# Optimization experiments

Measured on AMD Instinct MI355X. Metric: run time of the kernel, lower is better.

Reference implementation:

```python
import jax, jax.numpy as jnp
import numpy as np

VOCAB, EMB, HID, LAT = 32000, 512, 1024, 512
B, T = 32, 128


def setup_inputs() -> dict:
    key = jax.random.key(0)
    ks = jax.random.split(key, 10)
    s = 0.02
    return {
        "latent_vector": jax.random.normal(ks[0], (B, LAT), jnp.float32),
        "target_tokens": jax.random.randint(ks[1], (B, T), 0, VOCAB),
        "emb": jax.random.normal(ks[2], (VOCAB, EMB), jnp.float32) * s,
        "W_lh": jax.random.normal(ks[3], (HID, LAT), jnp.float32) * s,
        "b_lh": jnp.zeros((HID,), jnp.float32),
        "W_ih": jax.random.normal(ks[4], (4 * HID, EMB), jnp.float32) * s,
        "b_ih": jnp.zeros((4 * HID,), jnp.float32),
        "W_hh": jax.random.normal(ks[5], (4 * HID, HID), jnp.float32) * s,
        "b_hh": jnp.zeros((4 * HID,), jnp.float32),
        "W_out": jax.random.normal(ks[6], (VOCAB, HID), jnp.float32) * s,
        "b_out": jnp.zeros((VOCAB,), jnp.float32),
    }


def reference(latent_vector, target_tokens, emb, W_lh, b_lh, W_ih, b_ih, W_hh, b_hh, W_out, b_out):
    # teacher_forcing_ratio = 1.0 (deterministic): input at step t is target_tokens[:, t-1]
    h = latent_vector @ W_lh.T + b_lh            # [B, HID]
    c = jnp.zeros_like(h)
    xs = emb[target_tokens[:, :-1]]              # [B, T-1, EMB]
    xs = jnp.swapaxes(xs, 0, 1)                  # [T-1, B, EMB]

    def step(carry, x):
        h, c = carry
        gates = x @ W_ih.T + b_ih + h @ W_hh.T + b_hh   # [B, 4*HID]
        i, f, g, o = jnp.split(gates, 4, axis=-1)       # PyTorch LSTM gate order
        c = jax.nn.sigmoid(f) * c + jax.nn.sigmoid(i) * jnp.tanh(g)
        h = jax.nn.sigmoid(o) * jnp.tanh(c)
        logits = h @ W_out.T + b_out                    # [B, VOCAB]
        return (h, c), logits

    _, logits = jax.lax.scan(step, (h, c), xs)          # [T-1, B, VOCAB]
    return jnp.swapaxes(logits, 0, 1)                   # [B, T-1, VOCAB]
```

## Files before the change

### kernel.cpp

```cpp
#include <hip/hip_runtime.h>
#include <cstdint>

typedef __bf16 bf16x8 __attribute__((ext_vector_type(8)));
typedef __bf16 bf16x4 __attribute__((ext_vector_type(4)));
typedef float  f32x4  __attribute__((ext_vector_type(4)));

#define VOCAB 32000
#define EMB   512
#define HID   1024
#define LAT   512
#define BATCH 32
#define TSTEP 127
#define MROWS 4064
#define MPAD  4096
#define G4    4096
#define NBLK  128
#define NTM   32
#define NTN   250
#define FSTRIDE 64

__device__ __forceinline__ float sigf(float x){ return 1.0f / (1.0f + __expf(-x)); }
__device__ __forceinline__ float tanhfast(float x){
    float ax = fabsf(x);
    float e  = __expf(-2.0f * ax);
    float t  = (1.0f - e) / (1.0f + e);
    return copysignf(t, x);
}

__device__ __forceinline__ void gll16(void* lds, const void* gsrc){
    __builtin_amdgcn_global_load_lds(
        (const __attribute__((address_space(1))) unsigned int*)gsrc,
        (__attribute__((address_space(3))) unsigned int*)lds,
        16, 0, 0);
}

__global__ __launch_bounds__(256) void init_kernel(
    const float* __restrict__ latent,
    const float* __restrict__ Wlh,
    const float* __restrict__ blh,
    __bf16* __restrict__ h0,
    __bf16* __restrict__ Hall,
    unsigned* __restrict__ flags,
    const float* __restrict__ Whh,
    __bf16* __restrict__ Whhb)
{
    if (blockIdx.x >= 128){
        const int n4 = G4 * HID / 4;
        for (int i = (blockIdx.x - 128) * 256 + threadIdx.x; i < n4; i += 64 * 256){
            float4 v = ((const float4*)Whh)[i];
            bf16x4 o = { (__bf16)v.x, (__bf16)v.y, (__bf16)v.z, (__bf16)v.w };
            ((bf16x4*)Whhb)[i] = o;
        }
        return;
    }
    if (blockIdx.x == 0 && threadIdx.x < NBLK)
        flags[threadIdx.x * FSTRIDE] = 0u;

    int id = blockIdx.x * 256 + threadIdx.x;
    int b = id >> 10, j = id & 1023;
    float s = blh[j];
    const float4* lr = (const float4*)(latent + (size_t)b * LAT);
    const float4* wr = (const float4*)(Wlh + (size_t)j * LAT);
    for (int k = 0; k < LAT / 4; ++k){
        float4 a = lr[k], w = wr[k];
        s += a.x * w.x + a.y * w.y + a.z * w.z + a.w * w.w;
    }
    h0[id] = (__bf16)s;
    Hall[(size_t)MROWS * HID + id] = (__bf16)0.0f;
}

__global__ __launch_bounds__(256) void gemm_xg(
    const float* __restrict__ emb,
    const float* __restrict__ Wih,
    const int*   __restrict__ tok,
    float*       __restrict__ xg,
    const float* __restrict__ bih,
    const float* __restrict__ bhh)
{
    __shared__ __bf16 As[2][128 * 32];
    __shared__ __bf16 Bs[2][128 * 32];

    const int tid  = threadIdx.x;
    const int wid  = tid >> 6, lane = tid & 63;
    const int tile_n = blockIdx.x, tile_m = blockIdx.y;
    const int wr = wid >> 1, wc = wid & 1;

    f32x4 acc[4][4] = {};

    auto stage = [&](int kt, int buf){
        #pragma unroll
        for (int j = 0; j < 2; ++j){
            const int slot = tid + j * 256;
            const int row  = slot >> 2;
            const int kb   = kt * 32 + (slot & 3) * 8;
            {
                const int brow = tile_n * 128 + row;
                const float4* p = (const float4*)(Wih + (size_t)brow * EMB + kb);
                float4 u = p[0], v = p[1];
                bf16x8 w = { (__bf16)u.x, (__bf16)u.y, (__bf16)u.z, (__bf16)u.w,
                             (__bf16)v.x, (__bf16)v.y, (__bf16)v.z, (__bf16)v.w };
                *(bf16x8*)&Bs[buf][row * 32 + (slot & 3) * 8] = w;
            }
            {
                int r = tile_m * 128 + row;
                int rc = (r < MROWS) ? r : (MROWS - 1);
                int token = tok[(rc & 31) * 128 + (rc >> 5)];
                const float4* p = (const float4*)(emb + (size_t)token * EMB + kb);
                float4 u = p[0], v = p[1];
                bf16x8 w = { (__bf16)u.x, (__bf16)u.y, (__bf16)u.z, (__bf16)u.w,
                             (__bf16)v.x, (__bf16)v.y, (__bf16)v.z, (__bf16)v.w };
                *(bf16x8*)&As[buf][row * 32 + (slot & 3) * 8] = w;
            }
        }
    };

    const int KT = EMB / 32;
    stage(0, 0);
    for (int kt = 0; kt < KT; ++kt){
        const int buf = kt & 1;
        __syncthreads();
        if (kt + 1 < KT) stage(kt + 1, buf ^ 1);
        const __bf16* Abuf = As[buf];
        const __bf16* Bbuf = Bs[buf];
        const int ar = lane & 15, ko = (lane >> 4) * 8;
        bf16x8 av[4], bv[4];
        #pragma unroll
        for (int m = 0; m < 4; ++m)
            av[m] = *(const bf16x8*)&Abuf[(wr * 64 + m * 16 + ar) * 32 + ko];
        #pragma unroll
        for (int n = 0; n < 4; ++n)
            bv[n] = *(const bf16x8*)&Bbuf[(wc * 64 + n * 16 + ar) * 32 + ko];
        #pragma unroll
        for (int m = 0; m < 4; ++m)
            #pragma unroll
            for (int n = 0; n < 4; ++n)
                acc[m][n] = __builtin_amdgcn_mfma_f32_16x16x32_bf16(av[m], bv[n], acc[m][n], 0, 0, 0);
    }

    const int r0 = tile_m * 128 + wr * 64 + ((lane >> 4) << 2);
    const int c0 = tile_n * 128 + wc * 64 + (lane & 15);
    #pragma unroll
    for (int m = 0; m < 4; ++m){
        #pragma unroll
        for (int n = 0; n < 4; ++n){
            const int col = c0 + n * 16;
            float badd = bih[col] + bhh[col];
            #pragma unroll
            for (int q = 0; q < 4; ++q){
                int row = r0 + m * 16 + q;
                xg[(size_t)row * G4 + col] = acc[m][n][q] + badd;
            }
        }
    }
}

template<int BF16B>
__global__ __launch_bounds__(256) void gemm_logits(
    const __bf16* __restrict__ A,
    const float*  __restrict__ Bf,
    const __bf16* __restrict__ Bb,
    float*        __restrict__ C,
    const float*  __restrict__ bias)
{
    __shared__ __bf16 As[2][128 * 32];
    __shared__ __bf16 Bs[2][128 * 32];

    const int tid  = threadIdx.x;
    const int wid  = tid >> 6, lane = tid & 63;
    const int bid = blockIdx.x;
    const int s   = (bid & 7) * (NTM * NTN / 8) + (bid >> 3);
    const int g   = s / (8 * NTN), rem = s % (8 * NTN);
    const int tile_m = g * 8 + (rem & 7);
    const int tile_n = rem >> 3;
    const int wr = wid >> 1, wc = wid & 1;

    f32x4 acc[4][4] = {};

    auto stage = [&](int kt, int buf){
        const int kb = kt * 32 + (lane & 3) * 8;
        #pragma unroll
        for (int c2 = 0; c2 < 2; ++c2){
            int rA = tile_m * 128 + c2 * 64 + wid * 16 + (lane >> 2);
            gll16(&As[buf][c2 * 2048 + wid * 512], A + (size_t)rA * HID + kb);
            if constexpr (BF16B){
                int rB = tile_n * 128 + c2 * 64 + wid * 16 + (lane >> 2);
                gll16(&Bs[buf][c2 * 2048 + wid * 512], Bb + (size_t)rB * HID + kb);
            }
        }
        if constexpr (!BF16B){
            #pragma unroll
            for (int j = 0; j < 2; ++j){
                const int slot = tid + j * 256;
                const int row  = slot >> 2;
                const int kb2  = kt * 32 + (slot & 3) * 8;
                const int brow = tile_n * 128 + row;
                const float4* p = (const float4*)(Bf + (size_t)brow * HID + kb2);
                float4 u = p[0], v = p[1];
                bf16x8 w = { (__bf16)u.x, (__bf16)u.y, (__bf16)u.z, (__bf16)u.w,
                             (__bf16)v.x, (__bf16)v.y, (__bf16)v.z, (__bf16)v.w };
                *(bf16x8*)&Bs[buf][row * 32 + (slot & 3) * 8] = w;
            }
        }
    };

    const int KT = HID / 32;
    stage(0, 0);
    for (int kt = 0; kt < KT; ++kt){
        const int buf = kt & 1;
        __syncthreads();
        if (kt + 1 < KT) stage(kt + 1, buf ^ 1);
        const __bf16* Abuf = As[buf];
        const __bf16* Bbuf = Bs[buf];
        const int ar = lane & 15, ko = (lane >> 4) * 8;
        bf16x8 av[4], bv[4];
        #pragma unroll
        for (int m = 0; m < 4; ++m)
            av[m] = *(const bf16x8*)&Abuf[(wr * 64 + m * 16 + ar) * 32 + ko];
        #pragma unroll
        for (int n = 0; n < 4; ++n)
            bv[n] = *(const bf16x8*)&Bbuf[(wc * 64 + n * 16 + ar) * 32 + ko];
        #pragma unroll
        for (int m = 0; m < 4; ++m)
            #pragma unroll
            for (int n = 0; n < 4; ++n)
                acc[m][n] = __builtin_amdgcn_mfma_f32_16x16x32_bf16(av[m], bv[n], acc[m][n], 0, 0, 0);
    }

    const int r0 = tile_m * 128 + wr * 64 + ((lane >> 4) << 2);
    const int c0 = tile_n * 128 + wc * 64 + (lane & 15);
    #pragma unroll
    for (int m = 0; m < 4; ++m){
        #pragma unroll
        for (int n = 0; n < 4; ++n){
            const int col = c0 + n * 16;
            float badd = bias[col];
            #pragma unroll
            for (int q = 0; q < 4; ++q){
                int row = r0 + m * 16 + q;
                if (row < MROWS){
                    int t = row >> 5, b = row & 31;
                    __builtin_nontemporal_store(acc[m][n][q] + badd,
                        &C[((size_t)b * TSTEP + t) * VOCAB + col]);
                }
            }
        }
    }
}

__global__ __launch_bounds__(256) void lstm_coop(
    const float*  __restrict__ xg,
    __bf16*       __restrict__ Hall,
    __bf16*       __restrict__ hbuf,
    const __bf16* __restrict__ Whhb,
    unsigned*     __restrict__ flags,
    const float*  __restrict__ Woutf,
    __bf16*       __restrict__ Woutb)
{
    if (blockIdx.x >= NBLK){
        if (Woutb){
            const int n4 = VOCAB * HID / 4;
            for (int i = (blockIdx.x - NBLK) * 256 + threadIdx.x; i < n4; i += NBLK * 256){
                float4 v = ((const float4*)Woutf)[i];
                bf16x4 o = { (__bf16)v.x, (__bf16)v.y, (__bf16)v.z, (__bf16)v.w };
                ((bf16x4*)Woutb)[i] = o;
            }
        }
        return;
    }

    __shared__ float lds_g[4 * 4 * 4 * 64];
    const int tid = threadIdx.x, wid = tid >> 6, lane = tid & 63;
    const int jb = blockIdx.x * 8;

    bf16x8 bfrag[2][8];
    {
        const int gl = lane & 15, ko = (lane >> 4) * 8;
        #pragma unroll
        for (int nt = 0; nt < 2; ++nt){
            int gg = nt * 16 + gl;
            const __bf16* base =
                Whhb + (size_t)((gg >> 3) * HID + jb + (gg & 7)) * HID + wid * 256 + ko;
            #pragma unroll
            for (int ks = 0; ks < 8; ++ks)
                bfrag[nt][ks] = *(const bf16x8*)(base + ks * 32);
        }
    }

    const int b2 = tid >> 2, up0 = (tid & 3) * 2;
    const int mt2 = b2 >> 4, r2 = b2 & 15, reg2 = r2 & 3, lb2 = (r2 >> 2) << 4;
    float cst[2] = {0.0f, 0.0f};

    const float* xq = xg + (size_t)b2 * G4 + jb + up0;
    float2 xv[4];
    if (tid < 128){
        #pragma unroll
        for (int g = 0; g < 4; ++g) xv[g] = *(const float2*)(xq + g * HID);
    }

    const size_t e0 = (size_t)(lane & 15) * HID + wid * 256 + (lane >> 4) * 8;

    for (int t = 0; t < TSTEP; ++t){
        const unsigned long long* hq =
            (const unsigned long long*)(hbuf + (size_t)(t & 1) * (BATCH * HID));
        union { unsigned long long q[2]; bf16x8 v; } xa[16];
        #pragma unroll
        for (int ks = 0; ks < 8; ++ks){
            size_t q0 = (e0 + (size_t)ks * 32) >> 2;
            size_t q1 = q0 + ((size_t)16 * HID >> 2);
            xa[ks].q[0]     = __hip_atomic_load(hq + q0,     __ATOMIC_RELAXED, __HIP_MEMORY_SCOPE_AGENT);
            xa[ks].q[1]     = __hip_atomic_load(hq + q0 + 1, __ATOMIC_RELAXED, __HIP_MEMORY_SCOPE_AGENT);
            xa[8 + ks].q[0] = __hip_atomic_load(hq + q1,     __ATOMIC_RELAXED, __HIP_MEMORY_SCOPE_AGENT);
            xa[8 + ks].q[1] = __hip_atomic_load(hq + q1 + 1, __ATOMIC_RELAXED, __HIP_MEMORY_SCOPE_AGENT);
        }
        f32x4 a00 = {}, a01 = {}, a10 = {}, a11 = {};
        #pragma unroll
        for (int ks = 0; ks < 8; ++ks){
            a00 = __builtin_amdgcn_mfma_f32_16x16x32_bf16(xa[ks].v,     bfrag[0][ks], a00, 0, 0, 0);
            a01 = __builtin_amdgcn_mfma_f32_16x16x32_bf16(xa[ks].v,     bfrag[1][ks], a01, 0, 0, 0);
            a10 = __builtin_amdgcn_mfma_f32_16x16x32_bf16(xa[8 + ks].v, bfrag[0][ks], a10, 0, 0, 0);
            a11 = __builtin_amdgcn_mfma_f32_16x16x32_bf16(xa[8 + ks].v, bfrag[1][ks], a11, 0, 0, 0);
        }
        #pragma unroll
        for (int q = 0; q < 4; ++q){
            lds_g[((0 * 4 + wid) * 4 + q) * 64 + lane] = a00[q];
            lds_g[((1 * 4 + wid) * 4 + q) * 64 + lane] = a01[q];
            lds_g[((2 * 4 + wid) * 4 + q) * 64 + lane] = a10[q];
            lds_g[((3 * 4 + wid) * 4 + q) * 64 + lane] = a11[q];
        }
        __syncthreads();

        unsigned pku = 0;
        if (tid < 128){
            const float* xn = xq + (size_t)(t + 1) * (BATCH * G4);
            float2 xnew[4];
            #pragma unroll
            for (int g = 0; g < 4; ++g) xnew[g] = *(const float2*)(xn + g * HID);

            float h2[2];
            #pragma unroll
            for (int du = 0; du < 2; ++du){
                int u2 = up0 + du;
                float gate[4];
                #pragma unroll
                for (int ty = 0; ty < 4; ++ty){
                    int gg = ty * 8 + u2;
                    int mtnt = mt2 * 2 + (gg >> 4);
                    int li = lb2 | (gg & 15);
                    float s = 0.0f;
                    #pragma unroll
                    for (int w = 0; w < 4; ++w)
                        s += lds_g[((mtnt * 4 + w) * 4 + reg2) * 64 + li];
                    gate[ty] = s;
                }
                float gi = gate[0] + ((du == 0) ? xv[0].x : xv[0].y);
                float gf = gate[1] + ((du == 0) ? xv[1].x : xv[1].y);
                float gc = gate[2] + ((du == 0) ? xv[2].x : xv[2].y);
                float go = gate[3] + ((du == 0) ? xv[3].x : xv[3].y);
                float c = sigf(gf) * cst[du] + sigf(gi) * tanhfast(gc);
                cst[du] = c;
                h2[du] = sigf(go) * tanhfast(c);
            }
            #pragma unroll
            for (int g = 0; g < 4; ++g) xv[g] = xnew[g];

            union { __bf16 h[2]; unsigned u; } pk;
            pk.h[0] = (__bf16)h2[0]; pk.h[1] = (__bf16)h2[1];
            pku = pk.u;
            unsigned* hw = (unsigned*)(hbuf + (size_t)((t + 1) & 1) * (BATCH * HID)
                                       + (size_t)b2 * HID + jb + up0);
            __hip_atomic_store(hw, pku, __ATOMIC_RELAXED, __HIP_MEMORY_SCOPE_AGENT);
        }

        if (t + 1 == TSTEP){
            if (tid < 128)
                *(unsigned*)(Hall + ((size_t)t * BATCH + b2) * HID + jb + up0) = pku;
            break;
        }

        __syncthreads();
        if (tid == 0)
            __hip_atomic_store(&flags[blockIdx.x * FSTRIDE], (unsigned)(t + 1),
                               __ATOMIC_RELAXED, __HIP_MEMORY_SCOPE_AGENT);
        if (tid < 128)
            *(unsigned*)(Hall + ((size_t)t * BATCH + b2) * HID + jb + up0) = pku;
        if (wid == 0){
            const unsigned tgt = (unsigned)(t + 1);
            for (;;){
                unsigned f0 = __hip_atomic_load(&flags[lane * FSTRIDE],
                                  __ATOMIC_RELAXED, __HIP_MEMORY_SCOPE_AGENT);
                unsigned f1 = __hip_atomic_load(&flags[(lane + 64) * FSTRIDE],
                                  __ATOMIC_RELAXED, __HIP_MEMORY_SCOPE_AGENT);
                if (f0 >= tgt && f1 >= tgt) break;
                __builtin_amdgcn_s_sleep(1);
            }
        }
        __syncthreads();
    }
}

extern "C" void kernel_launch(void* const* d_in, const int* in_sizes, int n_in,
                              void* d_out, int out_size, void* d_ws, size_t ws_size,
                              hipStream_t stream)
{
    const float* latent = (const float*)d_in[0];
    const int*   tokens = (const int*)d_in[1];
    const float* emb    = (const float*)d_in[2];
    const float* Wlh    = (const float*)d_in[3];
    const float* blh    = (const float*)d_in[4];
    const float* Wih    = (const float*)d_in[5];
    const float* bih    = (const float*)d_in[6];
    const float* Whh    = (const float*)d_in[7];
    const float* bhh    = (const float*)d_in[8];
    const float* Wout   = (const float*)d_in[9];
    const float* bout   = (const float*)d_in[10];
    float* out = (float*)d_out;

    const size_t xg_b   = (size_t)MPAD * G4 * 4;
    const size_t hall_b = (size_t)MPAD * HID * 2;
    const size_t whh_b  = (size_t)G4 * HID * 2;
    const size_t wout_b = (size_t)VOCAB * HID * 2;
    const size_t hb_b   = (size_t)2 * BATCH * HID * 2;
    const size_t cnt_b  = (size_t)NBLK * FSTRIDE * 4;

    char* p = (char*)d_ws;
    const bool wsA = ws_size >= xg_b + hall_b + whh_b + wout_b + hb_b + cnt_b;
    const bool wsB = ws_size >= hall_b + whh_b + wout_b + hb_b + cnt_b;

    float* xg;
    if (wsA){ xg = (float*)p; p += xg_b; }
    else    { xg = (float*)d_out; }
    __bf16* Hall = (__bf16*)p; p += hall_b;
    __bf16* Whhb = (__bf16*)p; p += whh_b;
    __bf16* Woutb = nullptr;
    if (wsA || wsB){ Woutb = (__bf16*)p; p += wout_b; }
    __bf16* hbuf = (__bf16*)p; p += hb_b;
    unsigned* flags = (unsigned*)p; p += cnt_b;

    init_kernel<<<dim3(192), dim3(256), 0, stream>>>(
        latent, Wlh, blh, hbuf, Hall, flags, Whh, Whhb);

    gemm_xg<<<dim3(G4 / 128, MPAD / 128), dim3(256), 0, stream>>>(
        emb, Wih, tokens, xg, bih, bhh);

    {
        const float*  xgc   = xg;
        __bf16*       hallp = Hall;
        __bf16*       hbp   = hbuf;
        const __bf16* whhp  = Whhb;
        unsigned*     flagp = flags;
        const float*  wof   = Wout;
        __bf16*       wob   = Woutb;
        void* args[] = { (void*)&xgc, (void*)&hallp, (void*)&hbp, (void*)&whhp,
                         (void*)&flagp, (void*)&wof, (void*)&wob };
        hipLaunchCooperativeKernel((void*)lstm_coop, dim3(2 * NBLK), dim3(256),
                                   args, 0, stream);
    }

    if (Woutb)
        gemm_logits<1><<<dim3(NTM * NTN), dim3(256), 0, stream>>>(
            Hall, (const float*)nullptr, Woutb, out, bout);
    else
        gemm_logits<0><<<dim3(NTM * NTN), dim3(256), 0, stream>>>(
            Hall, Wout, (const __bf16*)nullptr, out, bout);
}
```

Before: 1.214 ms.

## Add 256x256-tile 8-wave logits GEMM with 4-stage async LDS pipeline

Replaces the 128x128-tile logits GEMM with a 512-thread kernel computing 256x256 output tiles. It uses a 4-slot global_load_lds ring, split A/B staging interleaved with the MFMA phases, and s_setprio around the MFMA bursts. Blocks are remapped so that blocks sharing A row tiles are grouped, and output is written with nontemporal stores. The larger tiles raise arithmetic intensity and cut L2/HBM re-reads, at the cost of more registers, 64KB of LDS and a tail wave on 2000 blocks. The old kernel stays as a fallback if the launch fails.

```diff
diff --git a/kernel.cpp b/kernel.cpp
--- a/kernel.cpp
+++ b/kernel.cpp
@@ -33,6 +33,7 @@
         (__attribute__((address_space(3))) unsigned int*)lds,
         16, 0, 0);
 }
+__device__ __forceinline__ void bar(){ asm volatile("s_barrier" ::: "memory"); }
 
 __global__ __launch_bounds__(256) void init_kernel(
     const float* __restrict__ latent,
@@ -149,6 +150,113 @@
             for (int q = 0; q < 4; ++q){
                 int row = r0 + m * 16 + q;
                 xg[(size_t)row * G4 + col] = acc[m][n][q] + badd;
+            }
+        }
+    }
+}
+
+__global__ __launch_bounds__(512) void gemm_logits8(
+    const __bf16* __restrict__ A,
+    const __bf16* __restrict__ B,
+    float*        __restrict__ C,
+    const float*  __restrict__ bias)
+{
+    __shared__ __bf16 sA[4][256][32];
+    __shared__ __bf16 sB[4][256][32];
+
+    const int tid = threadIdx.x;
+    const int wid = tid >> 6, lane = tid & 63;
+    const int wm = wid >> 2, wn = wid & 3;
+
+    const int bid = blockIdx.x;
+    const int s   = (bid & 7) * 250 + (bid >> 3);
+    const int g   = s / 500, rem = s % 500;
+    const int tm  = g * 4 + (rem & 3);
+    const int tn  = rem >> 2;
+
+    const int sr  = tid >> 2;
+    const int scb = tid & 3;
+    const __bf16* gA = A + (size_t)(tm * 256 + sr) * HID + scb * 8;
+    const __bf16* gB = B + (size_t)(tn * 256 + sr) * HID + scb * 8;
+    char* const dA0 = (char*)&sA[0][0][0] + wid * 1024;
+    char* const dB0 = (char*)&sB[0][0][0] + wid * 1024;
+
+    auto stageA = [&](int kt){
+        const int sl = kt & 3;
+        gll16(dA0 + sl * 16384,        gA + (size_t)kt * 32);
+        gll16(dA0 + sl * 16384 + 8192, gA + (size_t)128 * HID + (size_t)kt * 32);
+    };
+    auto stageB = [&](int kt){
+        const int sl = kt & 3;
+        gll16(dB0 + sl * 16384,        gB + (size_t)kt * 32);
+        gll16(dB0 + sl * 16384 + 8192, gB + (size_t)128 * HID + (size_t)kt * 32);
+    };
+
+    f32x4 acc[8][4] = {};
+    const int fr = lane & 15, fk = (lane >> 4) * 8;
+
+    stageA(0); stageB(0); stageA(1); stageB(1); stageA(2); stageB(2);
+    asm volatile("s_waitcnt vmcnt(8)" ::: "memory");
+    bar();
+
+    const int KT = HID / 32;
+    bf16x8 bfr[4], afr[4];
+    for (int kt = 0; kt < KT; ++kt){
+        const int sl = kt & 3;
+        #pragma unroll
+        for (int nf = 0; nf < 4; ++nf)
+            bfr[nf] = *(const bf16x8*)&sB[sl][wn * 64 + nf * 16 + fr][fk];
+        #pragma unroll
+        for (int mf = 0; mf < 4; ++mf)
+            afr[mf] = *(const bf16x8*)&sA[sl][wm * 128 + mf * 16 + fr][fk];
+        if (kt + 3 < KT) stageA(kt + 3);
+        bar();
+        asm volatile("s_waitcnt lgkmcnt(0)" ::: "memory");
+        __builtin_amdgcn_sched_barrier(0);
+        __builtin_amdgcn_s_setprio(1);
+        #pragma unroll
+        for (int mf = 0; mf < 4; ++mf)
+            #pragma unroll
+            for (int nf = 0; nf < 4; ++nf)
+                acc[mf][nf] = __builtin_amdgcn_mfma_f32_16x16x32_bf16(
+                    afr[mf], bfr[nf], acc[mf][nf], 0, 0, 0);
+        __builtin_amdgcn_s_setprio(0);
+        bar();
+        #pragma unroll
+        for (int mf = 0; mf < 4; ++mf)
+            afr[mf] = *(const bf16x8*)&sA[sl][wm * 128 + (mf + 4) * 16 + fr][fk];
+        if (kt + 3 < KT) stageB(kt + 3);
+        bar();
+        asm volatile("s_waitcnt lgkmcnt(0)" ::: "memory");
+        __builtin_amdgcn_sched_barrier(0);
+        __builtin_amdgcn_s_setprio(1);
+        #pragma unroll
+        for (int mf = 0; mf < 4; ++mf)
+            #pragma unroll
+            for (int nf = 0; nf < 4; ++nf)
+                acc[mf + 4][nf] = __builtin_amdgcn_mfma_f32_16x16x32_bf16(
+                    afr[mf], bfr[nf], acc[mf + 4][nf], 0, 0, 0);
+        __builtin_amdgcn_s_setprio(0);
+        if (kt < KT - 3)       asm volatile("s_waitcnt vmcnt(8)" ::: "memory");
+        else if (kt == KT - 3) asm volatile("s_waitcnt vmcnt(4)" ::: "memory");
+        else if (kt == KT - 2) asm volatile("s_waitcnt vmcnt(0)" ::: "memory");
+        bar();
+    }
+
+    #pragma unroll
+    for (int mf = 0; mf < 8; ++mf){
+        #pragma unroll
+        for (int nf = 0; nf < 4; ++nf){
+            const int col = tn * 256 + wn * 64 + nf * 16 + fr;
+            const float badd = bias[col];
+            #pragma unroll
+            for (int q = 0; q < 4; ++q){
+                int row = tm * 256 + wm * 128 + mf * 16 + (lane >> 4) * 4 + q;
+                if (row < MROWS){
+                    int t = row >> 5, b = row & 31;
+                    __builtin_nontemporal_store(acc[mf][nf][q] + badd,
+                        &C[((size_t)b * TSTEP + t) * VOCAB + col]);
+                }
             }
         }
     }
@@ -456,10 +564,15 @@
                                    args, 0, stream);
     }
 
-    if (Woutb)
-        gemm_logits<1><<<dim3(NTM * NTN), dim3(256), 0, stream>>>(
-            Hall, (const float*)nullptr, Woutb, out, bout);
-    else
+    if (Woutb){
+        (void)hipGetLastError();
+        gemm_logits8<<<dim3(2000), dim3(512), 0, stream>>>(Hall, Woutb, out, bout);
+        if (hipGetLastError() != hipSuccess){
+            gemm_logits<1><<<dim3(NTM * NTN), dim3(256), 0, stream>>>(
+                Hall, (const float*)nullptr, Woutb, out, bout);
+        }
+    } else {
         gemm_logits<0><<<dim3(NTM * NTN), dim3(256), 0, stream>>>(
             Hall, Wout, (const __bf16*)nullptr, out, bout);
-}
+    }
+}
```

Result: no change. 1.223 ms (+0.8%).

## Halve LSTM recurrence blocks to 64×512 threads and vectorize logits epilogue stores

Applied to the files above, without the earlier changes.

The cooperative LSTM kernel now runs 64 worker blocks of 512 threads, each owning 16 hidden units, instead of 128 blocks of 256 threads owning 8. This halves the number of flags polled in the per-step grid barrier and lets each wave carry a shorter K slice, with an 8-way LDS reduction across waves. The logits GEMM swaps its MFMA operands so that each lane holds four consecutive columns, which allows 16-byte vector nontemporal stores and vector bias loads in place of scalar ones. The tradeoff is fewer CUs working on the recurrence and more reduction work per block.

```diff
diff --git a/kernel.cpp b/kernel.cpp
--- a/kernel.cpp
+++ b/kernel.cpp
@@ -14,7 +14,7 @@
 #define MROWS 4064
 #define MPAD  4096
 #define G4    4096
-#define NBLK  128
+#define NBLK2 64
 #define NTM   32
 #define NTN   250
 #define FSTRIDE 64
@@ -53,7 +53,7 @@
         }
         return;
     }
-    if (blockIdx.x == 0 && threadIdx.x < NBLK)
+    if (blockIdx.x == 0 && threadIdx.x < 128)
         flags[threadIdx.x * FSTRIDE] = 0u;
 
     int id = blockIdx.x * 256 + threadIdx.x;
@@ -223,31 +223,30 @@
         for (int m = 0; m < 4; ++m)
             #pragma unroll
             for (int n = 0; n < 4; ++n)
-                acc[m][n] = __builtin_amdgcn_mfma_f32_16x16x32_bf16(av[m], bv[n], acc[m][n], 0, 0, 0);
-    }
-
-    const int r0 = tile_m * 128 + wr * 64 + ((lane >> 4) << 2);
-    const int c0 = tile_n * 128 + wc * 64 + (lane & 15);
+                acc[m][n] = __builtin_amdgcn_mfma_f32_16x16x32_bf16(
+                    bv[n], av[m], acc[m][n], 0, 0, 0);
+    }
+
+    const int r0 = tile_m * 128 + wr * 64 + (lane & 15);
+    const int c0 = tile_n * 128 + wc * 64 + ((lane >> 4) << 2);
     #pragma unroll
     for (int m = 0; m < 4; ++m){
-        #pragma unroll
-        for (int n = 0; n < 4; ++n){
-            const int col = c0 + n * 16;
-            float badd = bias[col];
-            #pragma unroll
-            for (int q = 0; q < 4; ++q){
-                int row = r0 + m * 16 + q;
-                if (row < MROWS){
-                    int t = row >> 5, b = row & 31;
-                    __builtin_nontemporal_store(acc[m][n][q] + badd,
-                        &C[((size_t)b * TSTEP + t) * VOCAB + col]);
-                }
-            }
-        }
-    }
-}
-
-__global__ __launch_bounds__(256) void lstm_coop(
+        const int row = r0 + m * 16;
+        if (row < MROWS){
+            const int t = row >> 5, b = row & 31;
+            float* crow = &C[((size_t)b * TSTEP + t) * VOCAB];
+            #pragma unroll
+            for (int n = 0; n < 4; ++n){
+                const int col = c0 + n * 16;
+                const f32x4 bd = *(const f32x4*)&bias[col];
+                f32x4 v = acc[m][n] + bd;
+                __builtin_nontemporal_store(v, (f32x4*)&crow[col]);
+            }
+        }
+    }
+}
+
+__global__ __launch_bounds__(512) void lstm_coop(
     const float*  __restrict__ xg,
     __bf16*       __restrict__ Hall,
     __bf16*       __restrict__ hbuf,
@@ -256,10 +255,10 @@
     const float*  __restrict__ Woutf,
     __bf16*       __restrict__ Woutb)
 {
-    if (blockIdx.x >= NBLK){
+    if (blockIdx.x >= NBLK2){
         if (Woutb){
             const int n4 = VOCAB * HID / 4;
-            for (int i = (blockIdx.x - NBLK) * 256 + threadIdx.x; i < n4; i += NBLK * 256){
+            for (int i = (blockIdx.x - NBLK2) * 512 + threadIdx.x; i < n4; i += 192 * 512){
                 float4 v = ((const float4*)Woutf)[i];
                 bf16x4 o = { (__bf16)v.x, (__bf16)v.y, (__bf16)v.z, (__bf16)v.w };
                 ((bf16x4*)Woutb)[i] = o;
@@ -268,69 +267,69 @@
         return;
     }
 
-    __shared__ float lds_g[4 * 4 * 4 * 64];
+    __shared__ float lds_g[8 * 8 * 4 * 64];
     const int tid = threadIdx.x, wid = tid >> 6, lane = tid & 63;
-    const int jb = blockIdx.x * 8;
-
-    bf16x8 bfrag[2][8];
+    const int jb = blockIdx.x * 16;
+
+    bf16x8 bfrag[4][4];
     {
-        const int gl = lane & 15, ko = (lane >> 4) * 8;
-        #pragma unroll
-        for (int nt = 0; nt < 2; ++nt){
-            int gg = nt * 16 + gl;
+        const int un = lane & 15, ko = (lane >> 4) * 8;
+        #pragma unroll
+        for (int cf = 0; cf < 4; ++cf){
             const __bf16* base =
-                Whhb + (size_t)((gg >> 3) * HID + jb + (gg & 7)) * HID + wid * 256 + ko;
-            #pragma unroll
-            for (int ks = 0; ks < 8; ++ks)
-                bfrag[nt][ks] = *(const bf16x8*)(base + ks * 32);
-        }
-    }
-
-    const int b2 = tid >> 2, up0 = (tid & 3) * 2;
+                Whhb + ((size_t)cf * HID + jb + un) * HID + wid * 128 + ko;
+            #pragma unroll
+            for (int ks = 0; ks < 4; ++ks)
+                bfrag[cf][ks] = *(const bf16x8*)(base + ks * 32);
+        }
+    }
+
+    const int b2 = tid >> 3, up0 = (tid & 7) * 2;
     const int mt2 = b2 >> 4, r2 = b2 & 15, reg2 = r2 & 3, lb2 = (r2 >> 2) << 4;
     float cst[2] = {0.0f, 0.0f};
 
     const float* xq = xg + (size_t)b2 * G4 + jb + up0;
     float2 xv[4];
-    if (tid < 128){
+    if (tid < 256){
         #pragma unroll
         for (int g = 0; g < 4; ++g) xv[g] = *(const float2*)(xq + g * HID);
     }
 
-    const size_t e0 = (size_t)(lane & 15) * HID + wid * 256 + (lane >> 4) * 8;
+    const size_t e0 = (size_t)(lane & 15) * HID + wid * 128 + (lane >> 4) * 8;
 
     for (int t = 0; t < TSTEP; ++t){
         const unsigned long long* hq =
             (const unsigned long long*)(hbuf + (size_t)(t & 1) * (BATCH * HID));
-        union { unsigned long long q[2]; bf16x8 v; } xa[16];
-        #pragma unroll
-        for (int ks = 0; ks < 8; ++ks){
+        union { unsigned long long q[2]; bf16x8 v; } xa[8];
+        #pragma unroll
+        for (int ks = 0; ks < 4; ++ks){
             size_t q0 = (e0 + (size_t)ks * 32) >> 2;
             size_t q1 = q0 + ((size_t)16 * HID >> 2);
             xa[ks].q[0]     = __hip_atomic_load(hq + q0,     __ATOMIC_RELAXED, __HIP_MEMORY_SCOPE_AGENT);
             xa[ks].q[1]     = __hip_atomic_load(hq + q0 + 1, __ATOMIC_RELAXED, __HIP_MEMORY_SCOPE_AGENT);
-            xa[8 + ks].q[0] = __hip_atomic_load(hq + q1,     __ATOMIC_RELAXED, __HIP_MEMORY_SCOPE_AGENT);
-            xa[8 + ks].q[1] = __hip_atomic_load(hq + q1 + 1, __ATOMIC_RELAXED, __HIP_MEMORY_SCOPE_AGENT);
-        }
-        f32x4 a00 = {}, a01 = {}, a10 = {}, a11 = {};
-        #pragma unroll
-        for (int ks = 0; ks < 8; ++ks){
-            a00 = __builtin_amdgcn_mfma_f32_16x16x32_bf16(xa[ks].v,     bfrag[0][ks], a00, 0, 0, 0);
-            a01 = __builtin_amdgcn_mfma_f32_16x16x32_bf16(xa[ks].v,     bfrag[1][ks], a01, 0, 0, 0);
-            a10 = __builtin_amdgcn_mfma_f32_16x16x32_bf16(xa[8 + ks].v, bfrag[0][ks], a10, 0, 0, 0);
-            a11 = __builtin_amdgcn_mfma_f32_16x16x32_bf16(xa[8 + ks].v, bfrag[1][ks], a11, 0, 0, 0);
-        }
-        #pragma unroll
-        for (int q = 0; q < 4; ++q){
-            lds_g[((0 * 4 + wid) * 4 + q) * 64 + lane] = a00[q];
-            lds_g[((1 * 4 + wid) * 4 + q) * 64 + lane] = a01[q];
-            lds_g[((2 * 4 + wid) * 4 + q) * 64 + lane] = a10[q];
-            lds_g[((3 * 4 + wid) * 4 + q) * 64 + lane] = a11[q];
-        }
+            xa[4 + ks].q[0] = __hip_atomic_load(hq + q1,     __ATOMIC_RELAXED, __HIP_MEMORY_SCOPE_AGENT);
+            xa[4 + ks].q[1] = __hip_atomic_load(hq + q1 + 1, __ATOMIC_RELAXED, __HIP_MEMORY_SCOPE_AGENT);
+        }
+        f32x4 a[2][4] = {};
+        #pragma unroll
+        for (int ks = 0; ks < 4; ++ks){
+            #pragma unroll
+            for (int cf = 0; cf < 4; ++cf){
+                a[0][cf] = __builtin_amdgcn_mfma_f32_16x16x32_bf16(xa[ks].v,     bfrag[cf][ks], a[0][cf], 0, 0, 0);
+                a[1][cf] = __builtin_amdgcn_mfma_f32_16x16x32_bf16(xa[4 + ks].v, bfrag[cf][ks], a[1][cf], 0, 0, 0);
+            }
+        }
+        #pragma unroll
+        for (int bh = 0; bh < 2; ++bh)
+            #pragma unroll
+            for (int cf = 0; cf < 4; ++cf)
+                #pragma unroll
+                for (int q = 0; q < 4; ++q)
+                    lds_g[((((bh * 4 + cf) * 8 + wid) * 4) + q) * 64 + lane] = a[bh][cf][q];
         __syncthreads();
 
         unsigned pku = 0;
-        if (tid < 128){
+        if (tid < 256){
             const float* xn = xq + (size_t)(t + 1) * (BATCH * G4);
             float2 xnew[4];
             #pragma unroll
@@ -343,13 +342,11 @@
                 float gate[4];
                 #pragma unroll
                 for (int ty = 0; ty < 4; ++ty){
-                    int gg = ty * 8 + u2;
-                    int mtnt = mt2 * 2 + (gg >> 4);
-                    int li = lb2 | (gg & 15);
+                    int li = lb2 | u2;
                     float s = 0.0f;
                     #pragma unroll
-                    for (int w = 0; w < 4; ++w)
-                        s += lds_g[((mtnt * 4 + w) * 4 + reg2) * 64 + li];
+                    for (int w = 0; w < 8; ++w)
+                        s += lds_g[((((mt2 * 4 + ty) * 8 + w) * 4) + reg2) * 64 + li];
                     gate[ty] = s;
                 }
                 float gi = gate[0] + ((du == 0) ? xv[0].x : xv[0].y);
@@ -372,7 +369,7 @@
         }
 
         if (t + 1 == TSTEP){
-            if (tid < 128)
+            if (tid < 256)
                 *(unsigned*)(Hall + ((size_t)t * BATCH + b2) * HID + jb + up0) = pku;
             break;
         }
@@ -381,16 +378,14 @@
         if (tid == 0)
             __hip_atomic_store(&flags[blockIdx.x * FSTRIDE], (unsigned)(t + 1),
                                __ATOMIC_RELAXED, __HIP_MEMORY_SCOPE_AGENT);
-        if (tid < 128)
+        if (tid < 256)
             *(unsigned*)(Hall + ((size_t)t * BATCH + b2) * HID + jb + up0) = pku;
         if (wid == 0){
             const unsigned tgt = (unsigned)(t + 1);
             for (;;){
                 unsigned f0 = __hip_atomic_load(&flags[lane * FSTRIDE],
                                   __ATOMIC_RELAXED, __HIP_MEMORY_SCOPE_AGENT);
-                unsigned f1 = __hip_atomic_load(&flags[(lane + 64) * FSTRIDE],
-                                  __ATOMIC_RELAXED, __HIP_MEMORY_SCOPE_AGENT);
-                if (f0 >= tgt && f1 >= tgt) break;
+                if (f0 >= tgt) break;
                 __builtin_amdgcn_s_sleep(1);
             }
         }
@@ -420,7 +415,7 @@
     const size_t whh_b  = (size_t)G4 * HID * 2;
     const size_t wout_b = (size_t)VOCAB * HID * 2;
     const size_t hb_b   = (size_t)2 * BATCH * HID * 2;
-    const size_t cnt_b  = (size_t)NBLK * FSTRIDE * 4;
+    const size_t cnt_b  = (size_t)128 * FSTRIDE * 4;
 
     char* p = (char*)d_ws;
     const bool wsA = ws_size >= xg_b + hall_b + whh_b + wout_b + hb_b + cnt_b;
@@ -452,8 +447,8 @@
         __bf16*       wob   = Woutb;
         void* args[] = { (void*)&xgc, (void*)&hallp, (void*)&hbp, (void*)&whhp,
                          (void*)&flagp, (void*)&wof, (void*)&wob };
-        hipLaunchCooperativeKernel((void*)lstm_coop, dim3(2 * NBLK), dim3(256),
-                                   args, 0, stream);
+        (void)hipLaunchCooperativeKernel((void*)lstm_coop, dim3(256), dim3(512),
+                                         args, 0, stream);
     }
 
     if (Woutb)
```

Result: no change. 1.210 ms (-0.3%).
